# Kernel tuning notes

Hardware: AMD Instinct MI355X
Metric: run time of the kernel (lower is better)

## Reference

```python
import math
import jax, jax.numpy as jnp
import numpy as np

B, N, D, H, PREFIX = 2, 2048, 2048, 16, 512
HD = D // H
ROPE_BASE = 10000.0

def _rope(x):
    # x: [b, h, n, d]; rotate-half RoPE with positions 0..n-1
    d = x.shape[-1]
    n = x.shape[-2]
    inv_freq = 1.0 / (ROPE_BASE ** (jnp.arange(0, d, 2, dtype=jnp.float32) / d))  # [d/2]
    pos = jnp.arange(n, dtype=jnp.float32)
    freqs = pos[:, None] * inv_freq[None, :]            # [n, d/2]
    cos, sin = jnp.cos(freqs), jnp.sin(freqs)
    x1, x2 = x[..., : d // 2], x[..., d // 2 :]
    return jnp.concatenate([x1 * cos - x2 * sin, x2 * cos + x1 * sin], axis=-1).astype(x.dtype)

def setup_inputs() -> dict:
    key = jax.random.key(0)
    ks = jax.random.split(key, 6)
    x = jax.random.normal(ks[0], (B, N, D), dtype=jnp.float32)
    prefix_k = jax.random.normal(ks[1], (B, H, PREFIX, HD), dtype=jnp.float32)
    prefix_v = jax.random.normal(ks[2], (B, H, PREFIX, HD), dtype=jnp.float32)
    Wqkv = jax.random.normal(ks[3], (D, 3 * D), dtype=jnp.float32) * (D ** -0.5)
    bqkv = jnp.zeros((3 * D,), dtype=jnp.float32)
    Wff = jax.random.normal(ks[4], (D, D), dtype=jnp.float32) * (D ** -0.5)
    bff = jnp.zeros((D,), dtype=jnp.float32)
    # causal mask over current tokens; prefix (cache) columns fully visible
    causal = jnp.tril(jnp.ones((N, N), dtype=jnp.int32))
    mask = jnp.concatenate([jnp.ones((N, PREFIX), dtype=jnp.int32), causal], axis=1)[None, None]  # [1,1,N,N+PREFIX]
    return {"x": x, "mask": mask, "prefix_k": prefix_k, "prefix_v": prefix_v,
            "Wqkv": Wqkv, "bqkv": bqkv, "Wff": Wff, "bff": bff}

def reference(x, mask, prefix_k, prefix_v, Wqkv, bqkv, Wff, bff):
    b, n, d = x.shape
    h = prefix_k.shape[1]
    hd = d // h
    qkv = (x @ Wqkv + bqkv).reshape(b, n, 3, h, hd)      # 'b n (c h d)'
    qkv = jnp.transpose(qkv, (2, 0, 3, 1, 4))            # -> c b h n d
    q, k, v = qkv[0], qkv[1], qkv[2]
    k = jnp.concatenate([prefix_k, k], axis=2)           # [b,h,kt,hd]
    v = jnp.concatenate([prefix_v, v], axis=2)
    next_prefix_kv = jnp.stack([k, v])                   # cached BEFORE rope (as in source)
    q = _rope(q)
    k = _rope(k)
    scores = jnp.einsum('bhqd,bhkd->bhqk', q, k) / math.sqrt(hd)
    scores = jnp.where(mask == 0, jnp.finfo(scores.dtype).min, scores)
    probs = jax.nn.softmax(scores, axis=-1)              # dropout_prob=0.0 -> identity
    attn_o = jnp.einsum('bhqk,bhkd->bhqd', probs, v)
    attn_o = jnp.transpose(attn_o, (0, 2, 1, 3)).reshape(b, n, d)
    return attn_o @ Wff + bff, next_prefix_kv
```

## Files before the change

kernel.cpp:

```cpp
#include <hip/hip_runtime.h>
#include <hip/hip_bf16.h>
#include <stdint.h>

#define TPB 256

using f32x4 = __attribute__((ext_vector_type(4))) float;
using s16x8 = __attribute__((ext_vector_type(8))) short;
using s16x4 = __attribute__((ext_vector_type(4))) short;

__device__ __forceinline__ short f2bf(float f){
  union { float f; uint32_t u; } v; v.f = f;
  uint32_t u = v.u;
  uint32_t r = (u + 0x7fffu + ((u >> 16) & 1u)) >> 16;
  return (short)(uint16_t)r;
}
__device__ __forceinline__ float bf2f(short b){
  union { uint32_t u; float f; } v; v.u = ((uint32_t)(uint16_t)b) << 16;
  return v.f;
}
__device__ __forceinline__ f32x4 mfma16(s16x8 a, s16x8 b, f32x4 c){
  return __builtin_amdgcn_mfma_f32_16x16x32_bf16(a, b, c, 0, 0, 0);
}

#define AS1(p) ((const __attribute__((address_space(1))) void*)(p))
#define AS3(p) ((__attribute__((address_space(3))) void*)(p))

__global__ void k_cvt_bf16(const float* __restrict__ src, short* __restrict__ dst, int n8){
  int i = blockIdx.x * TPB + threadIdx.x;
  if (i >= n8) return;
  const float4* s4 = (const float4*)src;
  float4 a = s4[2*i], b = s4[2*i+1];
  s16x8 o;
  o[0]=f2bf(a.x); o[1]=f2bf(a.y); o[2]=f2bf(a.z); o[3]=f2bf(a.w);
  o[4]=f2bf(b.x); o[5]=f2bf(b.y); o[6]=f2bf(b.z); o[7]=f2bf(b.w);
  *(s16x8*)(dst + 8*(size_t)i) = o;
}

__global__ void k_trans_cvt(const float* __restrict__ W, short* __restrict__ WT, int K, int Nn){
  __shared__ float ls[32][33];
  int k0 = blockIdx.x * 32, n0 = blockIdx.y * 32;
  int c = threadIdx.x & 31, i = threadIdx.x >> 5;
#pragma unroll
  for (int rr = 0; rr < 4; rr++){
    int row = i*4 + rr;
    ls[row][c] = W[(size_t)(k0+row)*Nn + n0 + c];
  }
  __syncthreads();
#pragma unroll
  for (int rr = 0; rr < 4; rr++){
    int ro = i*4 + rr;
    WT[(size_t)(n0+ro)*K + k0 + c] = f2bf(ls[c][ro]);
  }
}

template<int EPI>
__global__ void __launch_bounds__(512, 2) k_gemm8(
    const short* __restrict__ A, const short* __restrict__ Bt,
    int Nn, int K,
    const float* __restrict__ bias,
    float* __restrict__ outp,
    float* __restrict__ kvout,
    short* __restrict__ qpre, short* __restrict__ kpre, short* __restrict__ vpre)
{
  __shared__ __align__(16) short As[3][16384];
  __shared__ __align__(16) short Bs[3][8192];
  const int tid = threadIdx.x;
  const int w = tid >> 6, l = tid & 63;
  const int lrow = l & 15, lg = l >> 4;
  const int wm = w >> 1, wn = w & 1;
  const int m0 = blockIdx.x << 8, n0 = blockIdx.y << 7;
  const int NT = K >> 6;

  f32x4 acc[4][4] = {};

#define STAGE_A(slot, t, j) do {                                             \
    int chunk = ((w*4 + (j)) << 6) + l;                                      \
    int row = chunk >> 3, cc = chunk & 7;                                    \
    __builtin_amdgcn_global_load_lds(                                        \
      AS1(A + (size_t)(m0+row)*K + (t)*64 + ((cc ^ (row&7)) << 3)),          \
      AS3(&As[slot][(w*4 + (j)) << 9]), 16, 0, 0);                           \
  } while(0)
#define STAGE_B(slot, t, j) do {                                             \
    int chunk = ((w*2 + (j)) << 6) + l;                                      \
    int row = chunk >> 3, cc = chunk & 7;                                    \
    __builtin_amdgcn_global_load_lds(                                        \
      AS1(Bt + (size_t)(n0+row)*K + (t)*64 + ((cc ^ (row&7)) << 3)),         \
      AS3(&Bs[slot][(w*2 + (j)) << 9]), 16, 0, 0);                           \
  } while(0)

  STAGE_A(0,0,0); STAGE_A(0,0,1); STAGE_A(0,0,2); STAGE_A(0,0,3);
  STAGE_B(0,0,0); STAGE_B(0,0,1);
  STAGE_A(1,1,0); STAGE_A(1,1,1); STAGE_A(1,1,2); STAGE_A(1,1,3);
  STAGE_B(1,1,0); STAGE_B(1,1,1);

  int slot = 0;
  for (int t = 0; t < NT; ++t){
    if (t < NT-1) asm volatile("s_waitcnt vmcnt(6)" ::: "memory");
    else          asm volatile("s_waitcnt vmcnt(0)" ::: "memory");
    __builtin_amdgcn_s_barrier();
    asm volatile("" ::: "memory");
    const int sslot = (slot == 0) ? 2 : slot - 1;
    const bool st = (t+2) < NT;
    const char* ab = (const char*)As[slot];
    const char* bb = (const char*)Bs[slot];

    s16x8 bfr[4][2];
#pragma unroll
    for (int ni = 0; ni < 4; ni++){
      int row = wn*64 + ni*16 + lrow;
#pragma unroll
      for (int ks = 0; ks < 2; ks++)
        bfr[ni][ks] = *(const s16x8*)(bb + row*128 + ((ks*64 + lg*16) ^ ((row&7)<<4)));
    }
    s16x8 af[2][2];
#pragma unroll
    for (int mi = 0; mi < 2; mi++){
      int row = wm*64 + mi*16 + lrow;
#pragma unroll
      for (int ks = 0; ks < 2; ks++)
        af[mi][ks] = *(const s16x8*)(ab + row*128 + ((ks*64 + lg*16) ^ ((row&7)<<4)));
    }
    if (st){ STAGE_A(sslot,t+2,0); STAGE_A(sslot,t+2,1); STAGE_B(sslot,t+2,0); }
    __builtin_amdgcn_s_setprio(1);
#pragma unroll
    for (int ks = 0; ks < 2; ks++)
#pragma unroll
      for (int mi = 0; mi < 2; mi++)
#pragma unroll
        for (int ni = 0; ni < 4; ni++)
          acc[mi][ni] = mfma16(af[mi][ks], bfr[ni][ks], acc[mi][ni]);
    __builtin_amdgcn_s_setprio(0);
    asm volatile("" ::: "memory");
    __builtin_amdgcn_s_barrier();
    asm volatile("" ::: "memory");

    s16x8 af2[2][2];
#pragma unroll
    for (int mi = 0; mi < 2; mi++){
      int row = wm*64 + (mi+2)*16 + lrow;
#pragma unroll
      for (int ks = 0; ks < 2; ks++)
        af2[mi][ks] = *(const s16x8*)(ab + row*128 + ((ks*64 + lg*16) ^ ((row&7)<<4)));
    }
    if (st){ STAGE_A(sslot,t+2,2); STAGE_A(sslot,t+2,3); STAGE_B(sslot,t+2,1); }
    __builtin_amdgcn_s_setprio(1);
#pragma unroll
    for (int ks = 0; ks < 2; ks++)
#pragma unroll
      for (int mi = 0; mi < 2; mi++)
#pragma unroll
        for (int ni = 0; ni < 4; ni++)
          acc[mi+2][ni] = mfma16(af2[mi][ks], bfr[ni][ks], acc[mi+2][ni]);
    __builtin_amdgcn_s_setprio(0);
    slot = (slot == 2) ? 0 : slot + 1;
  }
#undef STAGE_A
#undef STAGE_B

#pragma unroll
  for (int mi = 0; mi < 4; mi++){
#pragma unroll
    for (int ni = 0; ni < 4; ni++){
      const int c  = n0 + wn*64 + ni*16 + lrow;
      const int mb = m0 + wm*64 + mi*16 + lg*4;
      const float bv = bias[c];
      if (EPI == 1){
#pragma unroll
        for (int r = 0; r < 4; r++)
          outp[(size_t)(mb+r)*Nn + c] = acc[mi][ni][r] + bv;
      } else {
        const int s = c >> 11, h = (c >> 7) & 15, tt = c & 127;
#pragma unroll
        for (int r = 0; r < 4; r++){
          const int m = mb + r;
          const int b = m >> 11, n = m & 2047;
          const int bh = b*16 + h;
          const float val = acc[mi][ni][r] + bv;
          if (s == 0){
            qpre[((size_t)bh*2048 + n)*128 + tt] = f2bf(val);
          } else if (s == 1){
            kvout[((size_t)bh*2560 + 512 + n)*128 + tt] = val;
            kpre[((size_t)bh*2048 + n)*128 + tt] = f2bf(val);
          } else {
            kvout[(size_t)(32 + bh)*327680 + (size_t)(512 + n)*128 + tt] = val;
            vpre[((size_t)bh*2048 + n)*128 + tt] = f2bf(val);
          }
        }
      }
    }
  }
}

__global__ void k_rope_k_new(const short* __restrict__ kpre, short* __restrict__ kr){
  int gid = blockIdx.x * TPB + threadIdx.x;
  int jb = (gid & 7) * 8; size_t row = gid >> 3;
  int bh = (int)(row >> 11), n = (int)(row & 2047);
  int pos = 512 + n;
  s16x8 v1 = *(const s16x8*)&kpre[row*128 + jb];
  s16x8 v2 = *(const s16x8*)&kpre[row*128 + 64 + jb];
  s16x8 o1, o2;
#pragma unroll
  for (int e = 0; e < 8; e++){
    float invf = __expf((float)(jb + e) * (-9.210340371976184f/64.0f));
    float sn, cs; __sincosf((float)pos * invf, &sn, &cs);
    float x1 = bf2f(v1[e]), x2 = bf2f(v2[e]);
    o1[e] = f2bf(x1*cs - x2*sn);
    o2[e] = f2bf(x2*cs + x1*sn);
  }
  size_t drow = (size_t)bh*2560 + pos;
  *(s16x8*)&kr[drow*128 + jb]      = o1;
  *(s16x8*)&kr[drow*128 + 64 + jb] = o2;
}

__global__ void k_rope_k_prefix(const float* __restrict__ pk, float* __restrict__ kvout0,
                                short* __restrict__ kr){
  int gid = blockIdx.x * TPB + threadIdx.x;
  int jb = (gid & 7) * 8; size_t row = gid >> 3;
  int bh = (int)(row >> 9), p = (int)(row & 511);
  float4 a1 = *(const float4*)&pk[row*128 + jb];
  float4 a2 = *(const float4*)&pk[row*128 + jb + 4];
  float4 b1 = *(const float4*)&pk[row*128 + 64 + jb];
  float4 b2 = *(const float4*)&pk[row*128 + 64 + jb + 4];
  size_t orow = (size_t)bh*2560 + p;
  *(float4*)&kvout0[orow*128 + jb]          = a1;
  *(float4*)&kvout0[orow*128 + jb + 4]      = a2;
  *(float4*)&kvout0[orow*128 + 64 + jb]     = b1;
  *(float4*)&kvout0[orow*128 + 64 + jb + 4] = b2;
  float x1[8] = {a1.x,a1.y,a1.z,a1.w,a2.x,a2.y,a2.z,a2.w};
  float x2[8] = {b1.x,b1.y,b1.z,b1.w,b2.x,b2.y,b2.z,b2.w};
  s16x8 o1, o2;
#pragma unroll
  for (int e = 0; e < 8; e++){
    float invf = __expf((float)(jb + e) * (-9.210340371976184f/64.0f));
    float sn, cs; __sincosf((float)p * invf, &sn, &cs);
    o1[e] = f2bf(x1[e]*cs - x2[e]*sn);
    o2[e] = f2bf(x2[e]*cs + x1[e]*sn);
  }
  *(s16x8*)&kr[orow*128 + jb]      = o1;
  *(s16x8*)&kr[orow*128 + 64 + jb] = o2;
}

__global__ void k_v_prefix(const float* __restrict__ pv, float* __restrict__ kvout1,
                           short* __restrict__ vT){
  __shared__ float ls[32][129];
  int bh = blockIdx.x >> 4, pt = blockIdx.x & 15;
  int p0 = pt*32, tid = threadIdx.x;
#pragma unroll
  for (int i = 0; i < 16; i++){
    int idx = i*TPB + tid; int p = idx >> 7, t = idx & 127;
    float v = pv[((size_t)bh*512 + p0 + p)*128 + t];
    ls[p][t] = v;
    kvout1[((size_t)bh*2560 + p0 + p)*128 + t] = v;
  }
  __syncthreads();
#pragma unroll
  for (int i = 0; i < 16; i++){
    int idx = i*TPB + tid; int t = idx >> 5, p = idx & 31;
    vT[((size_t)bh*128 + t)*2560 + p0 + p] = f2bf(ls[p][t]);
  }
}

__global__ void k_v_new(const short* __restrict__ vpre, short* __restrict__ vT){
  __shared__ float ls[32][129];
  int bh = blockIdx.x >> 6, nt = blockIdx.x & 63;
  int n0 = nt*32, tid = threadIdx.x;
#pragma unroll
  for (int i = 0; i < 16; i++){
    int idx = i*TPB + tid; int p = idx >> 7, t = idx & 127;
    ls[p][t] = bf2f(vpre[((size_t)bh*2048 + n0 + p)*128 + t]);
  }
  __syncthreads();
#pragma unroll
  for (int i = 0; i < 16; i++){
    int idx = i*TPB + tid; int t = idx >> 5, p = idx & 31;
    vT[((size_t)bh*128 + t)*2560 + 512 + n0 + p] = f2bf(ls[p][t]);
  }
}

__global__ void __launch_bounds__(256, 1) k_attn(
    const short* __restrict__ qr, const short* __restrict__ kr,
    const short* __restrict__ vT, short* __restrict__ attno)
{
  __shared__ short Ks[2][64*128];
  __shared__ short VTs[2][128*64];
  __shared__ short Ps[4][32*64 + 64];
  const int bh = blockIdx.x;
  const int pA = blockIdx.y, pB = 15 - pA;
  const int nA = 10 + 2*pA, nTot = 50;
  const int tid = threadIdx.x, w = tid >> 6, l = tid & 63;
  const int lrow = l & 15, lg = l >> 4;
  const int b = bh >> 4, h = bh & 15;

  s16x8 qfA[2][4], qfB[2][4];
  {
    const float sc = 0.088388347648318447f;
#pragma unroll
    for (int qb = 0; qb < 2; qb++){
      const int nAr = pA*128 + w*32 + qb*16 + lrow;
      const int nBr = pB*128 + w*32 + qb*16 + lrow;
      const size_t rA = (size_t)bh*2048 + nAr;
      const size_t rB = (size_t)bh*2048 + nBr;
#pragma unroll
      for (int ks = 0; ks < 4; ks++){
        qfA[qb][ks] = *(const s16x8*)&qr[rA*128 + ks*32 + lg*8];
        qfB[qb][ks] = *(const s16x8*)&qr[rB*128 + ks*32 + lg*8];
      }
#pragma unroll
      for (int ks = 0; ks < 2; ks++){
#pragma unroll
        for (int e = 0; e < 8; e++){
          const int j = ks*32 + lg*8 + e;
          const float invf = __expf((float)j * (-9.210340371976184f/64.0f));
          float sn, cs;
          __sincosf((float)nAr * invf, &sn, &cs);
          float x1 = bf2f(qfA[qb][ks][e]), x2 = bf2f(qfA[qb][ks+2][e]);
          qfA[qb][ks][e]   = f2bf((x1*cs - x2*sn) * sc);
          qfA[qb][ks+2][e] = f2bf((x2*cs + x1*sn) * sc);
          __sincosf((float)nBr * invf, &sn, &cs);
          float y1 = bf2f(qfB[qb][ks][e]), y2 = bf2f(qfB[qb][ks+2][e]);
          qfB[qb][ks][e]   = f2bf((y1*cs - y2*sn) * sc);
          qfB[qb][ks+2][e] = f2bf((y2*cs + y1*sn) * sc);
        }
      }
    }
  }

#define STAGE_KV(buf, kv0s) do {                                                    \
    _Pragma("unroll")                                                               \
    for (int i_ = 0; i_ < 4; i_++){                                                 \
      int chunk = i_*256 + tid;                                                     \
      int row = chunk >> 4, cc = (chunk & 15) ^ (row & 7);                          \
      __builtin_amdgcn_global_load_lds(                                             \
        AS1(kr + ((size_t)bh*2560 + (kv0s) + row)*128 + cc*8),                      \
        AS3((char*)Ks[buf] + (i_*256 + w*64)*16), 16, 0, 0);                        \
    }                                                                               \
    _Pragma("unroll")                                                               \
    for (int i_ = 0; i_ < 4; i_++){                                                 \
      int chunk = i_*256 + tid;                                                     \
      int row = chunk >> 3, cc = (chunk & 7) ^ (row & 7);                           \
      __builtin_amdgcn_global_load_lds(                                             \
        AS1(vT + ((size_t)bh*128 + row)*2560 + (kv0s) + cc*8),                      \
        AS3((char*)VTs[buf] + (i_*256 + w*64)*16), 16, 0, 0);                       \
    }                                                                               \
  } while(0)

  STAGE_KV(0, 0);
  STAGE_KV(1, 64);

  char* psw = (char*)&Ps[w][0];
  int g = 0;
#pragma unroll 2
  for (int ph = 0; ph < 2; ph++){
    const int qt = ph ? pB : pA;
    const int n = 10 + 2*qt;
    const int qbw = qt*128 + w*32;
    f32x4 acc0[8] = {}, acc1[8] = {};
    float mr0 = -1e30f, ls0 = 0.f;
    float mr1 = -1e30f, ls1 = 0.f;

    for (int t = 0; t < n; t++, g++){
      if (g+1 < nTot) asm volatile("s_waitcnt vmcnt(8)" ::: "memory");
      else            asm volatile("s_waitcnt vmcnt(0)" ::: "memory");
      __builtin_amdgcn_s_barrier();
      asm volatile("" ::: "memory");
      const char* kb_ = (const char*)Ks[g&1];
      const char* vb_ = (const char*)VTs[g&1];
      const int kv0 = t*64;

      f32x4 sf0[4], sf1[4];
      __builtin_amdgcn_s_setprio(1);
#pragma unroll
      for (int kb = 0; kb < 4; kb++){
        f32x4 s0 = {0.f,0.f,0.f,0.f}, s1 = {0.f,0.f,0.f,0.f};
#pragma unroll
        for (int ks = 0; ks < 4; ks++){
          int row  = kb*16 + lrow;
          int colb = ks*64 + lg*16;
          s16x8 kf = *(const s16x8*)(kb_ + row*256 + (colb ^ ((row&7)<<4)));
          s0 = mfma16(kf, ph ? qfB[0][ks] : qfA[0][ks], s0);
          s1 = mfma16(kf, ph ? qfB[1][ks] : qfA[1][ks], s1);
        }
        sf0[kb] = s0; sf1[kb] = s1;
      }
      __builtin_amdgcn_s_setprio(0);

      if (kv0 + 63 > 512 + qbw){
        const int qme0 = 512 + qbw + lrow;
        const int qme1 = qme0 + 16;
#pragma unroll
        for (int kb = 0; kb < 4; kb++)
#pragma unroll
          for (int r = 0; r < 4; r++){
            int kg = kv0 + kb*16 + lg*4 + r;
            if (kg > qme0) sf0[kb][r] = -1e30f;
            if (kg > qme1) sf1[kb][r] = -1e30f;
          }
      }

      {
        float m_ = fmaxf(
            fmaxf(fmaxf(fmaxf(sf0[0][0],sf0[0][1]),fmaxf(sf0[0][2],sf0[0][3])),
                  fmaxf(fmaxf(sf0[1][0],sf0[1][1]),fmaxf(sf0[1][2],sf0[1][3]))),
            fmaxf(fmaxf(fmaxf(sf0[2][0],sf0[2][1]),fmaxf(sf0[2][2],sf0[2][3])),
                  fmaxf(fmaxf(sf0[3][0],sf0[3][1]),fmaxf(sf0[3][2],sf0[3][3]))));
        m_ = fmaxf(m_, __shfl_xor(m_, 16));
        m_ = fmaxf(m_, __shfl_xor(m_, 32));
        if (__any(m_ > mr0 + 8.f)){
          float mnew = fmaxf(mr0, m_);
          float sc = __expf(mr0 - mnew);
          mr0 = mnew; ls0 *= sc;
          float scr[4];
#pragma unroll
          for (int r = 0; r < 4; r++)
            scr[r] = __shfl(sc, (l & 48) | (lg*4 + r));
#pragma unroll
          for (int dt = 0; dt < 8; dt++)
#pragma unroll
            for (int r = 0; r < 4; r++) acc0[dt][r] *= scr[r];
        }
#pragma unroll
        for (int kb = 0; kb < 4; kb++){
          float p0 = __expf(sf0[kb][0] - mr0);
          float p1 = __expf(sf0[kb][1] - mr0);
          float p2 = __expf(sf0[kb][2] - mr0);
          float p3 = __expf(sf0[kb][3] - mr0);
          ls0 += (p0+p1)+(p2+p3);
          s16x4 pk4 = { f2bf(p0), f2bf(p1), f2bf(p2), f2bf(p3) };
          *(s16x4*)(psw + (lrow*128 + ((kb*32 + lg*8) ^ ((lrow&7)<<4)))) = pk4;
        }
      }
      {
        float m_ = fmaxf(
            fmaxf(fmaxf(fmaxf(sf1[0][0],sf1[0][1]),fmaxf(sf1[0][2],sf1[0][3])),
                  fmaxf(fmaxf(sf1[1][0],sf1[1][1]),fmaxf(sf1[1][2],sf1[1][3]))),
            fmaxf(fmaxf(fmaxf(sf1[2][0],sf1[2][1]),fmaxf(sf1[2][2],sf1[2][3])),
                  fmaxf(fmaxf(sf1[3][0],sf1[3][1]),fmaxf(sf1[3][2],sf1[3][3]))));
        m_ = fmaxf(m_, __shfl_xor(m_, 16));
        m_ = fmaxf(m_, __shfl_xor(m_, 32));
        if (__any(m_ > mr1 + 8.f)){
          float mnew = fmaxf(mr1, m_);
          float sc = __expf(mr1 - mnew);
          mr1 = mnew; ls1 *= sc;
          float scr[4];
#pragma unroll
          for (int r = 0; r < 4; r++)
            scr[r] = __shfl(sc, (l & 48) | (lg*4 + r));
#pragma unroll
          for (int dt = 0; dt < 8; dt++)
#pragma unroll
            for (int r = 0; r < 4; r++) acc1[dt][r] *= scr[r];
        }
#pragma unroll
        for (int kb = 0; kb < 4; kb++){
          float p0 = __expf(sf1[kb][0] - mr1);
          float p1 = __expf(sf1[kb][1] - mr1);
          float p2 = __expf(sf1[kb][2] - mr1);
          float p3 = __expf(sf1[kb][3] - mr1);
          ls1 += (p0+p1)+(p2+p3);
          s16x4 pk4 = { f2bf(p0), f2bf(p1), f2bf(p2), f2bf(p3) };
          *(s16x4*)(psw + ((16 + lrow)*128 + ((kb*32 + lg*8) ^ ((lrow&7)<<4)))) = pk4;
        }
      }

      __builtin_amdgcn_s_setprio(1);
#pragma unroll
      for (int kp = 0; kp < 2; kp++){
        s16x8 pa0 = *(const s16x8*)(psw + (lrow*128       + ((kp*64 + lg*16) ^ ((lrow&7)<<4))));
        s16x8 pa1 = *(const s16x8*)(psw + ((16+lrow)*128  + ((kp*64 + lg*16) ^ ((lrow&7)<<4))));
#pragma unroll
        for (int dt = 0; dt < 8; dt++){
          int vrow = dt*16 + lrow;
          int vcolb = kp*64 + lg*16;
          s16x8 vf = *(const s16x8*)(vb_ + vrow*128 + (vcolb ^ ((vrow&7)<<4)));
          acc0[dt] = mfma16(pa0, vf, acc0[dt]);
          acc1[dt] = mfma16(pa1, vf, acc1[dt]);
        }
      }
      __builtin_amdgcn_s_setprio(0);

      asm volatile("" ::: "memory");
      __builtin_amdgcn_s_barrier();
      asm volatile("" ::: "memory");
      const int gg = g + 2;
      if (gg < nTot){
        const int kvs = (gg < nA ? gg : gg - nA) * 64;
        STAGE_KV(g&1, kvs);
      }
    }

    float lsa = ls0;
    lsa += __shfl_xor(lsa, 16);
    lsa += __shfl_xor(lsa, 32);
    float lsb = ls1;
    lsb += __shfl_xor(lsb, 16);
    lsb += __shfl_xor(lsb, 32);
    float linv0[4], linv1[4];
#pragma unroll
    for (int r = 0; r < 4; r++){
      linv0[r] = 1.f / __shfl(lsa, (l & 48) | (lg*4 + r));
      linv1[r] = 1.f / __shfl(lsb, (l & 48) | (lg*4 + r));
    }
#pragma unroll
    for (int dt = 0; dt < 8; dt++){
#pragma unroll
      for (int r = 0; r < 4; r++){
        const int dcol = h*128 + dt*16 + lrow;
        const int nrow0 = qbw + lg*4 + r;
        const int nrow1 = qbw + 16 + lg*4 + r;
        attno[((size_t)b*2048 + nrow0)*2048 + dcol] = f2bf(acc0[dt][r] * linv0[r]);
        attno[((size_t)b*2048 + nrow1)*2048 + dcol] = f2bf(acc1[dt][r] * linv1[r]);
      }
    }
  }
#undef STAGE_KV
}

extern "C" void kernel_launch(void* const* d_in, const int* in_sizes, int n_in,
                              void* d_out, int out_size, void* d_ws, size_t ws_size,
                              hipStream_t stream)
{
  const float* x    = (const float*)d_in[0];
  const float* pk   = (const float*)d_in[2];
  const float* pv   = (const float*)d_in[3];
  const float* Wqkv = (const float*)d_in[4];
  const float* bqkv = (const float*)d_in[5];
  const float* Wff  = (const float*)d_in[6];
  const float* bff  = (const float*)d_in[7];
  float* out   = (float*)d_out;
  float* kvout = out + 8388608;

  char* ws = (char*)d_ws;
  short* xb    = (short*)(ws);
  short* wqkvT = (short*)(ws + 16777216);
  short* wffT  = (short*)(ws + 41943040);
  short* qpre  = (short*)(ws + 50331648);
  short* kpre  = (short*)(ws + 67108864);
  short* vpre  = (short*)(ws + 83886080);
  short* krp   = (short*)(ws + 117440512);
  short* vTp   = (short*)(ws + 138412032);
  short* attno = (short*)(ws + 159383552);

  k_cvt_bf16<<<4096, TPB, 0, stream>>>(x, xb, 1048576);
  k_trans_cvt<<<dim3(64, 192), TPB, 0, stream>>>(Wqkv, wqkvT, 2048, 6144);
  k_trans_cvt<<<dim3(64, 64),  TPB, 0, stream>>>(Wff,  wffT,  2048, 2048);

  k_gemm8<0><<<dim3(16, 48), 512, 0, stream>>>(xb, wqkvT, 6144, 2048, bqkv,
                                               nullptr, kvout, qpre, kpre, vpre);

  k_rope_k_new<<<2048, TPB, 0, stream>>>(kpre, krp);
  k_rope_k_prefix<<<512, TPB, 0, stream>>>(pk, kvout, krp);
  k_v_prefix<<<512, TPB, 0, stream>>>(pv, kvout + (size_t)32*327680, vTp);
  k_v_new<<<2048, TPB, 0, stream>>>(vpre, vTp);

  k_attn<<<dim3(32, 8), 256, 0, stream>>>(qpre, krp, vTp, attno);

  k_gemm8<1><<<dim3(16, 16), 512, 0, stream>>>(attno, wffT, 2048, 2048, bff,
                                               out, nullptr, nullptr, nullptr, nullptr);
}
```

Baseline: 329.9 us.

## Split paired-tile attention blocks into one q-tile per block, two blocks per CU

Each attention block previously processed two complementary causal q-tiles (pA and 15-pA) in sequence so the work per block was balanced. Now each block handles a single 128-row q-tile, the grid doubles to 512 blocks, and launch bounds allow two blocks per CU, with the heaviest tiles scheduled first. This trades explicit load balancing for more parallelism and occupancy to hide latency. It risks register pressure from the occupancy bound and an uneven tail.

```diff
diff --git a/kernel.cpp b/kernel.cpp
--- a/kernel.cpp
+++ b/kernel.cpp
@@ -277,34 +277,31 @@
   }
 }
 
-__global__ void __launch_bounds__(256, 1) k_attn(
+__global__ void __launch_bounds__(256, 2) k_attn(
     const short* __restrict__ qr, const short* __restrict__ kr,
     const short* __restrict__ vT, short* __restrict__ attno)
 {
   __shared__ short Ks[2][64*128];
   __shared__ short VTs[2][128*64];
-  __shared__ short Ps[4][32*64 + 64];
+  __shared__ short Ps[4][32*64];
   const int bh = blockIdx.x;
-  const int pA = blockIdx.y, pB = 15 - pA;
-  const int nA = 10 + 2*pA, nTot = 50;
+  const int qt = 15 - (int)blockIdx.y;
+  const int n = 10 + 2*qt;
   const int tid = threadIdx.x, w = tid >> 6, l = tid & 63;
   const int lrow = l & 15, lg = l >> 4;
   const int b = bh >> 4, h = bh & 15;
-
-  s16x8 qfA[2][4], qfB[2][4];
+  const int qbw = qt*128 + w*32;
+
+  s16x8 qf[2][4];
   {
     const float sc = 0.088388347648318447f;
 #pragma unroll
     for (int qb = 0; qb < 2; qb++){
-      const int nAr = pA*128 + w*32 + qb*16 + lrow;
-      const int nBr = pB*128 + w*32 + qb*16 + lrow;
-      const size_t rA = (size_t)bh*2048 + nAr;
-      const size_t rB = (size_t)bh*2048 + nBr;
-#pragma unroll
-      for (int ks = 0; ks < 4; ks++){
-        qfA[qb][ks] = *(const s16x8*)&qr[rA*128 + ks*32 + lg*8];
-        qfB[qb][ks] = *(const s16x8*)&qr[rB*128 + ks*32 + lg*8];
-      }
+      const int nr = qbw + qb*16 + lrow;
+      const size_t rr = (size_t)bh*2048 + nr;
+#pragma unroll
+      for (int ks = 0; ks < 4; ks++)
+        qf[qb][ks] = *(const s16x8*)&qr[rr*128 + ks*32 + lg*8];
 #pragma unroll
       for (int ks = 0; ks < 2; ks++){
 #pragma unroll
@@ -312,14 +309,10 @@
           const int j = ks*32 + lg*8 + e;
           const float invf = __expf((float)j * (-9.210340371976184f/64.0f));
           float sn, cs;
-          __sincosf((float)nAr * invf, &sn, &cs);
-          float x1 = bf2f(qfA[qb][ks][e]), x2 = bf2f(qfA[qb][ks+2][e]);
-          qfA[qb][ks][e]   = f2bf((x1*cs - x2*sn) * sc);
-          qfA[qb][ks+2][e] = f2bf((x2*cs + x1*sn) * sc);
-          __sincosf((float)nBr * invf, &sn, &cs);
-          float y1 = bf2f(qfB[qb][ks][e]), y2 = bf2f(qfB[qb][ks+2][e]);
-          qfB[qb][ks][e]   = f2bf((y1*cs - y2*sn) * sc);
-          qfB[qb][ks+2][e] = f2bf((y2*cs + y1*sn) * sc);
+          __sincosf((float)nr * invf, &sn, &cs);
+          float x1 = bf2f(qf[qb][ks][e]), x2 = bf2f(qf[qb][ks+2][e]);
+          qf[qb][ks][e]   = f2bf((x1*cs - x2*sn) * sc);
+          qf[qb][ks+2][e] = f2bf((x2*cs + x1*sn) * sc);
         }
       }
     }
@@ -348,168 +341,157 @@
   STAGE_KV(1, 64);
 
   char* psw = (char*)&Ps[w][0];
-  int g = 0;
-#pragma unroll 2
-  for (int ph = 0; ph < 2; ph++){
-    const int qt = ph ? pB : pA;
-    const int n = 10 + 2*qt;
-    const int qbw = qt*128 + w*32;
-    f32x4 acc0[8] = {}, acc1[8] = {};
-    float mr0 = -1e30f, ls0 = 0.f;
-    float mr1 = -1e30f, ls1 = 0.f;
-
-    for (int t = 0; t < n; t++, g++){
-      if (g+1 < nTot) asm volatile("s_waitcnt vmcnt(8)" ::: "memory");
-      else            asm volatile("s_waitcnt vmcnt(0)" ::: "memory");
-      __builtin_amdgcn_s_barrier();
-      asm volatile("" ::: "memory");
-      const char* kb_ = (const char*)Ks[g&1];
-      const char* vb_ = (const char*)VTs[g&1];
-      const int kv0 = t*64;
-
-      f32x4 sf0[4], sf1[4];
-      __builtin_amdgcn_s_setprio(1);
+  f32x4 acc0[8] = {}, acc1[8] = {};
+  float mr0 = -1e30f, ls0 = 0.f;
+  float mr1 = -1e30f, ls1 = 0.f;
+
+  for (int t = 0; t < n; t++){
+    if (t+1 < n) asm volatile("s_waitcnt vmcnt(8)" ::: "memory");
+    else         asm volatile("s_waitcnt vmcnt(0)" ::: "memory");
+    __builtin_amdgcn_s_barrier();
+    asm volatile("" ::: "memory");
+    const char* kb_ = (const char*)Ks[t&1];
+    const char* vb_ = (const char*)VTs[t&1];
+    const int kv0 = t*64;
+
+    f32x4 sf0[4], sf1[4];
+    __builtin_amdgcn_s_setprio(1);
+#pragma unroll
+    for (int kb = 0; kb < 4; kb++){
+      f32x4 s0 = {0.f,0.f,0.f,0.f}, s1 = {0.f,0.f,0.f,0.f};
+#pragma unroll
+      for (int ks = 0; ks < 4; ks++){
+        int row  = kb*16 + lrow;
+        int colb = ks*64 + lg*16;
+        s16x8 kf = *(const s16x8*)(kb_ + row*256 + (colb ^ ((row&7)<<4)));
+        s0 = mfma16(kf, qf[0][ks], s0);
+        s1 = mfma16(kf, qf[1][ks], s1);
+      }
+      sf0[kb] = s0; sf1[kb] = s1;
+    }
+    __builtin_amdgcn_s_setprio(0);
+
+    if (kv0 + 63 > 512 + qbw){
+      const int qme0 = 512 + qbw + lrow;
+      const int qme1 = qme0 + 16;
+#pragma unroll
+      for (int kb = 0; kb < 4; kb++)
+#pragma unroll
+        for (int r = 0; r < 4; r++){
+          int kg = kv0 + kb*16 + lg*4 + r;
+          if (kg > qme0) sf0[kb][r] = -1e30f;
+          if (kg > qme1) sf1[kb][r] = -1e30f;
+        }
+    }
+
+    {
+      float m_ = fmaxf(
+          fmaxf(fmaxf(fmaxf(sf0[0][0],sf0[0][1]),fmaxf(sf0[0][2],sf0[0][3])),
+                fmaxf(fmaxf(sf0[1][0],sf0[1][1]),fmaxf(sf0[1][2],sf0[1][3]))),
+          fmaxf(fmaxf(fmaxf(sf0[2][0],sf0[2][1]),fmaxf(sf0[2][2],sf0[2][3])),
+                fmaxf(fmaxf(sf0[3][0],sf0[3][1]),fmaxf(sf0[3][2],sf0[3][3]))));
+      m_ = fmaxf(m_, __shfl_xor(m_, 16));
+      m_ = fmaxf(m_, __shfl_xor(m_, 32));
+      if (__any(m_ > mr0 + 8.f)){
+        float mnew = fmaxf(mr0, m_);
+        float sc = __expf(mr0 - mnew);
+        mr0 = mnew; ls0 *= sc;
+        float scr[4];
+#pragma unroll
+        for (int r = 0; r < 4; r++)
+          scr[r] = __shfl(sc, (l & 48) | (lg*4 + r));
+#pragma unroll
+        for (int dt = 0; dt < 8; dt++)
+#pragma unroll
+          for (int r = 0; r < 4; r++) acc0[dt][r] *= scr[r];
+      }
 #pragma unroll
       for (int kb = 0; kb < 4; kb++){
-        f32x4 s0 = {0.f,0.f,0.f,0.f}, s1 = {0.f,0.f,0.f,0.f};
-#pragma unroll
-        for (int ks = 0; ks < 4; ks++){
-          int row  = kb*16 + lrow;
-          int colb = ks*64 + lg*16;
-          s16x8 kf = *(const s16x8*)(kb_ + row*256 + (colb ^ ((row&7)<<4)));
-          s0 = mfma16(kf, ph ? qfB[0][ks] : qfA[0][ks], s0);
-          s1 = mfma16(kf, ph ? qfB[1][ks] : qfA[1][ks], s1);
-        }
-        sf0[kb] = s0; sf1[kb] = s1;
-      }
-      __builtin_amdgcn_s_setprio(0);
-
-      if (kv0 + 63 > 512 + qbw){
-        const int qme0 = 512 + qbw + lrow;
-        const int qme1 = qme0 + 16;
-#pragma unroll
-        for (int kb = 0; kb < 4; kb++)
-#pragma unroll
-          for (int r = 0; r < 4; r++){
-            int kg = kv0 + kb*16 + lg*4 + r;
-            if (kg > qme0) sf0[kb][r] = -1e30f;
-            if (kg > qme1) sf1[kb][r] = -1e30f;
-          }
-      }
-
-      {
-        float m_ = fmaxf(
-            fmaxf(fmaxf(fmaxf(sf0[0][0],sf0[0][1]),fmaxf(sf0[0][2],sf0[0][3])),
-                  fmaxf(fmaxf(sf0[1][0],sf0[1][1]),fmaxf(sf0[1][2],sf0[1][3]))),
-            fmaxf(fmaxf(fmaxf(sf0[2][0],sf0[2][1]),fmaxf(sf0[2][2],sf0[2][3])),
-                  fmaxf(fmaxf(sf0[3][0],sf0[3][1]),fmaxf(sf0[3][2],sf0[3][3]))));
-        m_ = fmaxf(m_, __shfl_xor(m_, 16));
-        m_ = fmaxf(m_, __shfl_xor(m_, 32));
-        if (__any(m_ > mr0 + 8.f)){
-          float mnew = fmaxf(mr0, m_);
-          float sc = __expf(mr0 - mnew);
-          mr0 = mnew; ls0 *= sc;
-          float scr[4];
-#pragma unroll
-          for (int r = 0; r < 4; r++)
-            scr[r] = __shfl(sc, (l & 48) | (lg*4 + r));
-#pragma unroll
-          for (int dt = 0; dt < 8; dt++)
-#pragma unroll
-            for (int r = 0; r < 4; r++) acc0[dt][r] *= scr[r];
-        }
-#pragma unroll
-        for (int kb = 0; kb < 4; kb++){
-          float p0 = __expf(sf0[kb][0] - mr0);
-          float p1 = __expf(sf0[kb][1] - mr0);
-          float p2 = __expf(sf0[kb][2] - mr0);
-          float p3 = __expf(sf0[kb][3] - mr0);
-          ls0 += (p0+p1)+(p2+p3);
-          s16x4 pk4 = { f2bf(p0), f2bf(p1), f2bf(p2), f2bf(p3) };
-          *(s16x4*)(psw + (lrow*128 + ((kb*32 + lg*8) ^ ((lrow&7)<<4)))) = pk4;
-        }
-      }
-      {
-        float m_ = fmaxf(
-            fmaxf(fmaxf(fmaxf(sf1[0][0],sf1[0][1]),fmaxf(sf1[0][2],sf1[0][3])),
-                  fmaxf(fmaxf(sf1[1][0],sf1[1][1]),fmaxf(sf1[1][2],sf1[1][3]))),
-            fmaxf(fmaxf(fmaxf(sf1[2][0],sf1[2][1]),fmaxf(sf1[2][2],sf1[2][3])),
-                  fmaxf(fmaxf(sf1[3][0],sf1[3][1]),fmaxf(sf1[3][2],sf1[3][3]))));
-        m_ = fmaxf(m_, __shfl_xor(m_, 16));
-        m_ = fmaxf(m_, __shfl_xor(m_, 32));
-        if (__any(m_ > mr1 + 8.f)){
-          float mnew = fmaxf(mr1, m_);
-          float sc = __expf(mr1 - mnew);
-          mr1 = mnew; ls1 *= sc;
-          float scr[4];
-#pragma unroll
-          for (int r = 0; r < 4; r++)
-            scr[r] = __shfl(sc, (l & 48) | (lg*4 + r));
-#pragma unroll
-          for (int dt = 0; dt < 8; dt++)
-#pragma unroll
-            for (int r = 0; r < 4; r++) acc1[dt][r] *= scr[r];
-        }
-#pragma unroll
-        for (int kb = 0; kb < 4; kb++){
-          float p0 = __expf(sf1[kb][0] - mr1);
-          float p1 = __expf(sf1[kb][1] - mr1);
-          float p2 = __expf(sf1[kb][2] - mr1);
-          float p3 = __expf(sf1[kb][3] - mr1);
-          ls1 += (p0+p1)+(p2+p3);
-          s16x4 pk4 = { f2bf(p0), f2bf(p1), f2bf(p2), f2bf(p3) };
-          *(s16x4*)(psw + ((16 + lrow)*128 + ((kb*32 + lg*8) ^ ((lrow&7)<<4)))) = pk4;
-        }
-      }
-
-      __builtin_amdgcn_s_setprio(1);
-#pragma unroll
-      for (int kp = 0; kp < 2; kp++){
-        s16x8 pa0 = *(const s16x8*)(psw + (lrow*128       + ((kp*64 + lg*16) ^ ((lrow&7)<<4))));
-        s16x8 pa1 = *(const s16x8*)(psw + ((16+lrow)*128  + ((kp*64 + lg*16) ^ ((lrow&7)<<4))));
-#pragma unroll
-        for (int dt = 0; dt < 8; dt++){
-          int vrow = dt*16 + lrow;
-          int vcolb = kp*64 + lg*16;
-          s16x8 vf = *(const s16x8*)(vb_ + vrow*128 + (vcolb ^ ((vrow&7)<<4)));
-          acc0[dt] = mfma16(pa0, vf, acc0[dt]);
-          acc1[dt] = mfma16(pa1, vf, acc1[dt]);
-        }
-      }
-      __builtin_amdgcn_s_setprio(0);
-
-      asm volatile("" ::: "memory");
-      __builtin_amdgcn_s_barrier();
-      asm volatile("" ::: "memory");
-      const int gg = g + 2;
-      if (gg < nTot){
-        const int kvs = (gg < nA ? gg : gg - nA) * 64;
-        STAGE_KV(g&1, kvs);
-      }
-    }
-
-    float lsa = ls0;
-    lsa += __shfl_xor(lsa, 16);
-    lsa += __shfl_xor(lsa, 32);
-    float lsb = ls1;
-    lsb += __shfl_xor(lsb, 16);
-    lsb += __shfl_xor(lsb, 32);
-    float linv0[4], linv1[4];
+        float p0 = __expf(sf0[kb][0] - mr0);
+        float p1 = __expf(sf0[kb][1] - mr0);
+        float p2 = __expf(sf0[kb][2] - mr0);
+        float p3 = __expf(sf0[kb][3] - mr0);
+        ls0 += (p0+p1)+(p2+p3);
+        s16x4 pk4 = { f2bf(p0), f2bf(p1), f2bf(p2), f2bf(p3) };
+        *(s16x4*)(psw + (lrow*128 + ((kb*32 + lg*8) ^ ((lrow&7)<<4)))) = pk4;
+      }
+    }
+    {
+      float m_ = fmaxf(
+          fmaxf(fmaxf(fmaxf(sf1[0][0],sf1[0][1]),fmaxf(sf1[0][2],sf1[0][3])),
+                fmaxf(fmaxf(sf1[1][0],sf1[1][1]),fmaxf(sf1[1][2],sf1[1][3]))),
+          fmaxf(fmaxf(fmaxf(sf1[2][0],sf1[2][1]),fmaxf(sf1[2][2],sf1[2][3])),
+                fmaxf(fmaxf(sf1[3][0],sf1[3][1]),fmaxf(sf1[3][2],sf1[3][3]))));
+      m_ = fmaxf(m_, __shfl_xor(m_, 16));
+      m_ = fmaxf(m_, __shfl_xor(m_, 32));
+      if (__any(m_ > mr1 + 8.f)){
+        float mnew = fmaxf(mr1, m_);
+        float sc = __expf(mr1 - mnew);
+        mr1 = mnew; ls1 *= sc;
+        float scr[4];
+#pragma unroll
+        for (int r = 0; r < 4; r++)
+          scr[r] = __shfl(sc, (l & 48) | (lg*4 + r));
+#pragma unroll
+        for (int dt = 0; dt < 8; dt++)
+#pragma unroll
+          for (int r = 0; r < 4; r++) acc1[dt][r] *= scr[r];
+      }
+#pragma unroll
+      for (int kb = 0; kb < 4; kb++){
+        float p0 = __expf(sf1[kb][0] - mr1);
+        float p1 = __expf(sf1[kb][1] - mr1);
+        float p2 = __expf(sf1[kb][2] - mr1);
+        float p3 = __expf(sf1[kb][3] - mr1);
+        ls1 += (p0+p1)+(p2+p3);
+        s16x4 pk4 = { f2bf(p0), f2bf(p1), f2bf(p2), f2bf(p3) };
+        *(s16x4*)(psw + ((16 + lrow)*128 + ((kb*32 + lg*8) ^ ((lrow&7)<<4)))) = pk4;
+      }
+    }
+
+    __builtin_amdgcn_s_setprio(1);
+#pragma unroll
+    for (int kp = 0; kp < 2; kp++){
+      s16x8 pa0 = *(const s16x8*)(psw + (lrow*128       + ((kp*64 + lg*16) ^ ((lrow&7)<<4))));
+      s16x8 pa1 = *(const s16x8*)(psw + ((16+lrow)*128  + ((kp*64 + lg*16) ^ ((lrow&7)<<4))));
+#pragma unroll
+      for (int dt = 0; dt < 8; dt++){
+        int vrow = dt*16 + lrow;
+        int vcolb = kp*64 + lg*16;
+        s16x8 vf = *(const s16x8*)(vb_ + vrow*128 + (vcolb ^ ((vrow&7)<<4)));
+        acc0[dt] = mfma16(pa0, vf, acc0[dt]);
+        acc1[dt] = mfma16(pa1, vf, acc1[dt]);
+      }
+    }
+    __builtin_amdgcn_s_setprio(0);
+
+    asm volatile("" ::: "memory");
+    __builtin_amdgcn_s_barrier();
+    asm volatile("" ::: "memory");
+    if (t + 2 < n) STAGE_KV(t&1, (t+2)*64);
+  }
+
+  float lsa = ls0;
+  lsa += __shfl_xor(lsa, 16);
+  lsa += __shfl_xor(lsa, 32);
+  float lsb = ls1;
+  lsb += __shfl_xor(lsb, 16);
+  lsb += __shfl_xor(lsb, 32);
+  float linv0[4], linv1[4];
+#pragma unroll
+  for (int r = 0; r < 4; r++){
+    linv0[r] = 1.f / __shfl(lsa, (l & 48) | (lg*4 + r));
+    linv1[r] = 1.f / __shfl(lsb, (l & 48) | (lg*4 + r));
+  }
+#pragma unroll
+  for (int dt = 0; dt < 8; dt++){
 #pragma unroll
     for (int r = 0; r < 4; r++){
-      linv0[r] = 1.f / __shfl(lsa, (l & 48) | (lg*4 + r));
-      linv1[r] = 1.f / __shfl(lsb, (l & 48) | (lg*4 + r));
-    }
-#pragma unroll
-    for (int dt = 0; dt < 8; dt++){
-#pragma unroll
-      for (int r = 0; r < 4; r++){
-        const int dcol = h*128 + dt*16 + lrow;
-        const int nrow0 = qbw + lg*4 + r;
-        const int nrow1 = qbw + 16 + lg*4 + r;
-        attno[((size_t)b*2048 + nrow0)*2048 + dcol] = f2bf(acc0[dt][r] * linv0[r]);
-        attno[((size_t)b*2048 + nrow1)*2048 + dcol] = f2bf(acc1[dt][r] * linv1[r]);
-      }
+      const int dcol = h*128 + dt*16 + lrow;
+      const int nrow0 = qbw + lg*4 + r;
+      const int nrow1 = qbw + 16 + lg*4 + r;
+      attno[((size_t)b*2048 + nrow0)*2048 + dcol] = f2bf(acc0[dt][r] * linv0[r]);
+      attno[((size_t)b*2048 + nrow1)*2048 + dcol] = f2bf(acc1[dt][r] * linv1[r]);
     }
   }
 #undef STAGE_KV
@@ -552,7 +534,7 @@
   k_v_prefix<<<512, TPB, 0, stream>>>(pv, kvout + (size_t)32*327680, vTp);
   k_v_new<<<2048, TPB, 0, stream>>>(vpre, vTp);
 
-  k_attn<<<dim3(32, 8), 256, 0, stream>>>(qpre, krp, vTp, attno);
+  k_attn<<<dim3(32, 16), 256, 0, stream>>>(qpre, krp, vTp, attno);
 
   k_gemm8<1><<<dim3(16, 16), 512, 0, stream>>>(attno, wffT, 2048, 2048, bff,
                                                out, nullptr, nullptr, nullptr, nullptr);
```

Result: faster. 306.8 us (-7.0%).
